# Kernel tuning notes

Measured on AMD Instinct MI355X. Metric: run time of the kernel, lower is better.

Reference implementation:

```python
import jax, jax.numpy as jnp
import numpy as np

B, G, GI = 128, 360, 174          # batch, n_groups, voxels per group
EF, ET, U = 512, 512, 512         # feat embed, text embed, LSTM units
AU, VOC, T = 32, 5000, 20         # attention units, vocab, max_len


def _leaky(x):
    return jnp.where(x >= 0, x, 0.2 * x)


def _ln(x, g, b, eps=1e-5):
    m = x.mean(-1, keepdims=True)
    v = ((x - m) ** 2).mean(-1, keepdims=True)
    return (x - m) / jnp.sqrt(v + eps) * g + b


def setup_inputs() -> dict:
    key = jax.random.key(0)
    ks = jax.random.split(key, 24)
    def n(k, shape, s=0.02):
        return jax.random.normal(k, shape, jnp.float32) * s
    return {
        "features": jax.random.normal(ks[0], (B, G * GI), jnp.float32),
        "text": jax.random.randint(ks[1], (B, T), 0, VOC),
        "a0": jnp.zeros((B, U), jnp.float32),
        "c0": jnp.zeros((B, U), jnp.float32),
        "enc_W": n(ks[2], (G, GI, EF)), "enc_b": n(ks[3], (G, EF)),
        "enc_ln_g": jnp.ones((EF,), jnp.float32), "enc_ln_b": jnp.zeros((EF,), jnp.float32),
        "attn_W1": n(ks[4], (EF, AU)), "attn_b1": n(ks[5], (AU,)),
        "attn_W2": n(ks[6], (U, AU)), "attn_b2": n(ks[7], (AU,)),
        "attn_V": n(ks[8], (AU, 1)), "attn_bV": n(ks[9], (1,)),
        "emb": n(ks[10], (VOC, ET)),
        "W_ih": n(ks[11], (4 * U, EF + ET)), "W_hh": n(ks[12], (4 * U, U)),
        "b_ih": n(ks[13], (4 * U,)), "b_hh": n(ks[14], (4 * U,)),
        "ln_g": jnp.ones((U,), jnp.float32), "ln_b": jnp.zeros((U,), jnp.float32),
        "dec_W1": n(ks[15], (U, 256)), "dec_b1": n(ks[16], (256,)),
        "dec_W2": n(ks[17], (256, VOC)), "dec_b2": n(ks[18], (VOC,)),
        "subject": 0,
    }


def reference(features, text, a0, c0, enc_W, enc_b, enc_ln_g, enc_ln_b,
              attn_W1, attn_b1, attn_W2, attn_b2, attn_V, attn_bV, emb,
              W_ih, W_hh, b_ih, b_hh, ln_g, ln_b,
              dec_W1, dec_b1, dec_W2, dec_b2, subject):
    # LocallyConnected encoder (weights for the selected subject): groups are
    # 360 contiguous equal splits of the voxel axis -> gather == reshape.
    x = features.reshape(B, G, GI)
    feat = _ln(_leaky(jnp.einsum('bgi,gio->bgo', x, enc_W) + enc_b),
               enc_ln_g, enc_ln_b)                       # [B, G, EF]
    # hidden-independent half of attention, hoisted out of the recurrence
    f1 = jax.nn.relu(jnp.einsum('bge,eu->bgu', feat, attn_W1) + attn_b1)  # [B,G,AU]
    txt = emb[text]                                      # [B, T, ET]

    def step(carry, x_t):
        a, c = carry                                     # [B,U], [B,U]
        h2 = jax.nn.relu(a @ attn_W2 + attn_b2)          # [B, AU]
        score = jnp.tanh(f1 + h2[:, None, :]) @ attn_V + attn_bV  # [B,G,1]
        w = jax.nn.softmax(score, axis=1)
        ctx = jnp.sum(w * feat, axis=1)                  # [B, EF]
        xin = jnp.concatenate([ctx, x_t], axis=1)        # [B, EF+ET]
        gates = xin @ W_ih.T + a @ W_hh.T + b_ih + b_hh  # [B, 4U]
        i, f, g, o = jnp.split(gates, 4, axis=1)         # torch gate order i,f,g,o
        c = jax.nn.sigmoid(f) * c + jax.nn.sigmoid(i) * jnp.tanh(g)
        h = jax.nn.sigmoid(o) * jnp.tanh(c)
        a = _ln(_leaky(h), ln_g, ln_b)                   # fed back as LSTM hidden
        out = jax.nn.softmax(_leaky(a @ dec_W1 + dec_b1) @ dec_W2 + dec_b2, axis=-1)
        return (a, c), (out, w)

    _, (outs, ws) = jax.lax.scan(step, (a0, c0), jnp.swapaxes(txt, 0, 1))
    output = jnp.swapaxes(outs, 0, 1)                    # [B, T, VOC]
    attention_scores = jnp.swapaxes(ws, 0, 1)            # [B, T, G, 1]
    return output, attention_scores
```

## Files before the change

### kernel.cpp

```cpp
#include <hip/hip_runtime.h>
#include <stdint.h>

#define B_  128
#define G_  360
#define GI_ 174
#define EF_ 512
#define U_  512
#define AU_ 32
#define VOC_ 5000
#define T_  20

typedef short short8 __attribute__((ext_vector_type(8)));
typedef float floatx4 __attribute__((ext_vector_type(4)));

#define GLD16(gp, lp) __builtin_amdgcn_global_load_lds( \
    (const __attribute__((address_space(1))) void*)(gp), \
    (__attribute__((address_space(3))) void*)(lp), 16, 0, 0)

__device__ __forceinline__ unsigned short f2bf(float f){
  unsigned u = __float_as_uint(f);
  u += 0x7fffu + ((u>>16)&1u);
  return (unsigned short)(u>>16);
}
__device__ __forceinline__ float2 bfpair(unsigned u){
  float2 r; r.x = __uint_as_float(u<<16); r.y = __uint_as_float(u & 0xffff0000u); return r;
}
__device__ __forceinline__ unsigned packbf(float a, float b){
  return ((unsigned)f2bf(b)<<16) | (unsigned)f2bf(a);
}
__device__ __forceinline__ float sigmf(float x){ return 1.0f/(1.0f + __expf(-x)); }
__device__ __forceinline__ float tanhf_(float x){ return 1.0f - 2.0f/(1.0f + __expf(2.0f*x)); }
__device__ __forceinline__ float leaky_(float x){ return x >= 0.f ? x : 0.2f*x; }

__device__ __forceinline__ int swzcol(int cc, int e){
  return (cc & ~63) | ((((cc>>3)&7) ^ e)<<3) | (cc&7);
}

__global__ __launch_bounds__(256) void k_cvt(
    const int* __restrict__ text, const float* __restrict__ emb,
    const float* __restrict__ Wih, const float* __restrict__ Whh,
    const float* __restrict__ bih, const float* __restrict__ bhh,
    const float* __restrict__ W1, const float* __restrict__ b1,
    const float* __restrict__ encg, const float* __restrict__ encb,
    const float* __restrict__ dW1, const float* __restrict__ dW2,
    float* __restrict__ stats, unsigned short* __restrict__ Wstep,
    float* __restrict__ bias_sum, unsigned short* __restrict__ ASbuf,
    unsigned short* __restrict__ W1g, float* __restrict__ f1c,
    unsigned short* __restrict__ dW1t, unsigned short* __restrict__ dW2t)
{
  __shared__ float tile[64][65];
  const int blk = blockIdx.x, tid = threadIdx.x;
  if (blk < 90){
    int i = blk*1024 + tid*4;
    *(float4*)&stats[i] = make_float4(0.f,0.f,0.f,0.f);
  } else if (blk < 2138){
    int j = blk - 90;
    #pragma unroll
    for (int q=0;q<6;++q){
      int c = q*256 + tid;
      float v;
      if (c < 512)       v = Wih[(size_t)j*1024 + 512 + c];
      else if (c < 1024) v = Wih[(size_t)j*1024 + (c - 512)];
      else               v = Whh[(size_t)j*512 + (c - 1024)];
      int cd = c;
      if (c >= 512) cd = 512 + swzcol(c - 512, j&7);
      Wstep[(size_t)j*1536 + cd] = f2bf(v);
    }
  } else if (blk < 2146){
    int i = (blk-2138)*256 + tid;
    bias_sum[i] = bih[i] + bhh[i];
  } else if (blk < 4706){
    int r = blk - 2146; int t = r >> 7, b = r & 127;
    int idx = text[b*T_ + t];
    float2 v = *(const float2*)&emb[(size_t)idx*512 + 2*tid];
    ((unsigned*)ASbuf)[(((size_t)r*1536)>>1) + tid] = packbf(v.x, v.y);
  } else if (blk == 4706){
    if (tid < 32){
      float gw = 0.f, bw = 0.f;
      for (int k=0;k<512;++k){
        float wv = W1[(size_t)k*32 + tid];
        float gk = encg[k], bk = encb[k];
        W1g[(size_t)tid*512 + k] = f2bf(gk*wv);
        gw += gk*wv; bw += bk*wv;
      }
      f1c[tid] = gw; f1c[32+tid] = bw + b1[tid];
    }
  } else if (blk < 4739){
    int q = blk - 4707; int kt = q >> 2, nt = q & 3;
    int k0 = kt*64, n0 = nt*64;
    #pragma unroll
    for (int it=0; it<16; ++it){
      int idx = it*256 + tid; int kk = idx>>6, nn = idx&63;
      tile[kk][nn] = dW1[(size_t)(k0+kk)*256 + n0+nn];
    }
    __syncthreads();
    #pragma unroll
    for (int it=0; it<16; ++it){
      int idx = it*256 + tid; int nn = idx>>6, kk = idx&63;
      dW1t[(size_t)(n0+nn)*512 + k0+kk] = f2bf(tile[kk][nn]);
    }
  } else {
    int q = blk - 4739; int kt = q/80, nt = q - kt*80;
    int k0 = kt*64, n0 = nt*64;
    #pragma unroll
    for (int it=0; it<16; ++it){
      int idx = it*256 + tid; int kk = idx>>6, nn = idx&63;
      tile[kk][nn] = (n0+nn < VOC_) ? dW2[(size_t)(k0+kk)*VOC_ + n0+nn] : 0.f;
    }
    __syncthreads();
    #pragma unroll
    for (int it=0; it<16; ++it){
      int idx = it*256 + tid; int nn = idx>>6, kk = idx&63;
      dW2t[(size_t)(n0+nn)*256 + k0+kk] = f2bf(tile[kk][nn]);
    }
  }
}

__device__ __forceinline__ int swz64(int row, int k){
  return row*64 + ((((k>>3) ^ (row&7)))<<3) + (k&7);
}
__global__ __launch_bounds__(256, 3) void k_enc(
    const float* __restrict__ features, const float* __restrict__ encW,
    const float* __restrict__ encB,
    unsigned short* __restrict__ ybuf, float* __restrict__ stats)
{
  __shared__ __align__(16) unsigned short As[128*64];
  __shared__ __align__(16) unsigned short Bs[128*64];
  const int g = blockIdx.y, n0 = blockIdx.x*128;
  const int tid = threadIdx.x, w = tid>>6, l = tid&63;
  const int quad = l>>4, col16 = l&15;
  const int m0w = (w>>1)*64, n0w = (w&1)*64;

  floatx4 acc[4][4];
  #pragma unroll
  for (int mi=0;mi<4;++mi)
    #pragma unroll
    for (int ni=0;ni<4;++ni)
      acc[mi][ni] = (floatx4){0.f,0.f,0.f,0.f};

  for (int c=0; c<3; ++c){
    if (c > 0) __syncthreads();
    #pragma unroll
    for (int q=0; q<8; ++q){
      int idx = q*256 + tid;
      int row = idx >> 4;
      int kq  = idx & 15;
      int kl  = kq*4;
      int kgl = c*64 + kl;
      const float* fp = features + (size_t)row*(G_*GI_) + (size_t)g*GI_ + kgl;
      float4 v;
      if (kgl + 3 < GI_){
        v = *(const float4*)fp;
      } else {
        v.x = (kgl+0 < GI_) ? fp[0] : 0.f;
        v.y = (kgl+1 < GI_) ? fp[1] : 0.f;
        v.z = (kgl+2 < GI_) ? fp[2] : 0.f;
        v.w = (kgl+3 < GI_) ? fp[3] : 0.f;
      }
      int e = row*64 + (((kl>>3) ^ (row&7))<<3) + (kl&7);
      uint2 pk; pk.x = packbf(v.x, v.y); pk.y = packbf(v.z, v.w);
      *(uint2*)&As[e] = pk;
    }
    #pragma unroll
    for (int zb=0; zb<2; ++zb){
      #pragma unroll
      for (int z=0; z<8; ++z){
        int zz = zb*8 + z;
        int kk = w + 4*zz;
        int k  = c*64 + kk;
        if (k < GI_){
          const float* wp = encW + ((size_t)g*GI_ + k)*512 + n0;
          float2 v = *(const float2*)&wp[2*l];
          Bs[swz64(2*l,   kk)] = f2bf(v.x);
          Bs[swz64(2*l+1, kk)] = f2bf(v.y);
        } else {
          Bs[swz64(2*l,   kk)] = 0;
          Bs[swz64(2*l+1, kk)] = 0;
        }
      }
    }
    __syncthreads();
    #pragma unroll
    for (int it=0; it<2; ++it){
      int kk = it*32 + quad*8;
      short8 af[4], bfr[4];
      #pragma unroll
      for (int mi=0;mi<4;++mi){
        int row = m0w + mi*16 + col16;
        af[mi] = *(const short8*)&As[row*64 + (((kk>>3) ^ (row&7))<<3)];
      }
      #pragma unroll
      for (int ni=0;ni<4;++ni){
        int rowb = n0w + ni*16 + col16;
        bfr[ni] = *(const short8*)&Bs[rowb*64 + (((kk>>3) ^ (rowb&7))<<3)];
      }
      #pragma unroll
      for (int mi=0;mi<4;++mi)
        #pragma unroll
        for (int ni=0;ni<4;++ni)
          acc[mi][ni] = __builtin_amdgcn_mfma_f32_16x16x32_bf16(af[mi], bfr[ni], acc[mi][ni], 0,0,0);
    }
  }

  #pragma unroll
  for (int mi=0;mi<4;++mi){
    float sy[4] = {0.f,0.f,0.f,0.f};
    float sq[4] = {0.f,0.f,0.f,0.f};
    #pragma unroll
    for (int ni=0;ni<4;++ni){
      int nG = n0 + n0w + ni*16 + col16;
      float bv = encB[(size_t)g*512 + nG];
      #pragma unroll
      for (int reg=0;reg<4;++reg){
        int row = m0w + mi*16 + quad*4 + reg;
        float y = leaky_(acc[mi][ni][reg] + bv);
        unsigned short yh = f2bf(y);
        ybuf[((size_t)row*G_ + g)*512 + nG] = yh;
        float yr = __uint_as_float(((unsigned)yh)<<16);
        sy[reg] += yr; sq[reg] += yr*yr;
      }
    }
    #pragma unroll
    for (int reg=0; reg<4; ++reg){
      float a = sy[reg], bq = sq[reg];
      #pragma unroll
      for (int mk=1; mk<16; mk<<=1){ a += __shfl_xor(a, mk, 64); bq += __shfl_xor(bq, mk, 64); }
      if (col16 == 0){
        int row = m0w + mi*16 + quad*4 + reg;
        atomicAdd(&stats[((size_t)row*G_ + g)*2],     a);
        atomicAdd(&stats[((size_t)row*G_ + g)*2 + 1], bq);
      }
    }
  }
}

template<int TN, int NBK, int MODE, int KSPLIT=1>
__global__ __launch_bounds__(256) void k_gemm(
    const unsigned short* __restrict__ A, int lda,
    const unsigned short* __restrict__ Bt, int ldb,
    const float* __restrict__ bias,
    float* __restrict__ outf, unsigned short* __restrict__ outh,
    const float* __restrict__ stats, float* __restrict__ stats2,
    const float* __restrict__ f1c)
{
  constexpr int NI = TN/32;
  __shared__ __align__(16) unsigned short As[128*64];
  __shared__ __align__(16) unsigned short Bs[TN*64];
  const int tid = threadIdx.x;
  const int w = tid >> 6, l = tid & 63;
  const int n0 = blockIdx.x * TN;
  const int ks = (KSPLIT > 1) ? blockIdx.y : 0;
  const int r0 = (KSPLIT > 1) ? 0 : blockIdx.y * 128;
  const int quad = l>>4, col16 = l&15;
  const int m0w = (w>>1)*64, n0w = (w&1)*(TN/2);
  const int arow = w*32, brow = w*(TN/4);

  const unsigned short* Ag = A + (size_t)(r0 + arow + (l>>3))*lda + (l&7)*8;
  const unsigned short* Bg = Bt + (size_t)(n0 + brow + (l>>3))*ldb + (l&7)*8;

  floatx4 acc[4][NI];
  #pragma unroll
  for (int mi=0;mi<4;++mi)
    #pragma unroll
    for (int ni=0;ni<NI;++ni)
      acc[mi][ni] = (floatx4){0.f,0.f,0.f,0.f};

  for (int it=0; it<NBK; ++it){
    int k0 = (ks*NBK + it)*64;
    #pragma unroll
    for (int q=0;q<4;++q)
      GLD16(Ag + (size_t)q*8*lda + k0, As + (arow + q*8)*64);
    #pragma unroll
    for (int q=0;q<TN/32;++q)
      GLD16(Bg + (size_t)q*8*ldb + k0, Bs + (brow + q*8)*64);
    __syncthreads();
    #pragma unroll
    for (int kc=0;kc<2;++kc){
      int koff = kc*32 + quad*8;
      short8 af[4], bfr[NI];
      #pragma unroll
      for (int mi=0;mi<4;++mi)
        af[mi] = *(const short8*)&As[(m0w + mi*16 + col16)*64 + koff];
      #pragma unroll
      for (int ni=0;ni<NI;++ni)
        bfr[ni] = *(const short8*)&Bs[(n0w + ni*16 + col16)*64 + koff];
      #pragma unroll
      for (int mi=0;mi<4;++mi)
        #pragma unroll
        for (int ni=0;ni<NI;++ni)
          acc[mi][ni] = __builtin_amdgcn_mfma_f32_16x16x32_bf16(af[mi], bfr[ni], acc[mi][ni], 0,0,0);
    }
    __syncthreads();
  }

  if constexpr (MODE == 0){
    float* op = outf + (size_t)ks*(128*2048);
    #pragma unroll
    for (int ni=0; ni<NI; ++ni){
      int nG = n0 + n0w + ni*16 + col16;
      float bv = (KSPLIT == 1 || ks == 0) ? bias[nG] : 0.f;
      #pragma unroll
      for (int mi=0; mi<4; ++mi)
        #pragma unroll
        for (int reg=0; reg<4; ++reg){
          int r = r0 + m0w + mi*16 + quad*4 + reg;
          op[(size_t)r*2048 + nG] = acc[mi][ni][reg] + bv;
        }
    }
  } else if constexpr (MODE == 1){
    int nG = n0w + col16;
    float gw = f1c[nG], bwv = f1c[32+nG];
    #pragma unroll
    for (int mi=0; mi<4; ++mi)
      #pragma unroll
      for (int reg=0; reg<4; ++reg){
        int r = r0 + m0w + mi*16 + quad*4 + reg;
        float2 st = *(const float2*)&stats[(size_t)r*2];
        float m = st.x * (1.f/512.f);
        float var = st.y * (1.f/512.f) - m*m;
        float rs = rsqrtf(var + 1e-5f);
        float v = rs*(acc[mi][0][reg] - m*gw) + bwv;
        v = v > 0.f ? v : 0.f;
        outf[(size_t)r*32 + nG] = v;
        if (((w&1)==0) && col16==0){
          stats2[(size_t)r*2] = m; stats2[(size_t)r*2+1] = rs;
        }
      }
  } else if constexpr (MODE == 2){
    #pragma unroll
    for (int ni=0; ni<NI; ++ni){
      int nG = n0 + n0w + ni*16 + col16;
      float bv = bias[nG];
      #pragma unroll
      for (int mi=0; mi<4; ++mi)
        #pragma unroll
        for (int reg=0; reg<4; ++reg){
          int r = r0 + m0w + mi*16 + quad*4 + reg;
          outh[(size_t)r*256 + nG] = f2bf(leaky_(acc[mi][ni][reg] + bv));
        }
    }
  } else {
    #pragma unroll
    for (int ni=0; ni<NI; ++ni){
      int nG = n0 + n0w + ni*16 + col16;
      if (nG < VOC_){
        float bv = bias[nG];
        #pragma unroll
        for (int mi=0; mi<4; ++mi)
          #pragma unroll
          for (int reg=0; reg<4; ++reg){
            int r = r0 + m0w + mi*16 + quad*4 + reg;
            int bb = r & 127, tt = r >> 7;
            outf[((size_t)bb*T_ + tt)*VOC_ + nG] = acc[mi][ni][reg] + bv;
          }
      }
    }
  }
}

__global__ __launch_bounds__(256) void k_gates(
    const unsigned short* __restrict__ A,
    const unsigned short* __restrict__ Bt,
    float* __restrict__ outp)
{
  __shared__ __align__(16) unsigned short As[128*128];
  __shared__ __align__(16) unsigned short Bs[64*128];
  const int tid = threadIdx.x, w = tid>>6, l = tid&63;
  const int ks = blockIdx.y;
  const int n0 = blockIdx.x*64;
  const int quad = l>>4, col16 = l&15;
  const int m0w = (w>>1)*64, n0w = (w&1)*32;
  const int arow = w*32, brow = w*16;

  const unsigned short* Ag = A + (size_t)(arow + (l>>4))*1536 + ks*128 + (l&15)*8;
  const unsigned short* Bg = Bt + (size_t)(n0 + brow + (l>>4))*1536 + 512 + ks*128 + (l&15)*8;
  #pragma unroll
  for (int q=0;q<8;++q)
    GLD16(Ag + (size_t)q*4*1536, As + (arow + q*4)*128);
  #pragma unroll
  for (int q=0;q<4;++q)
    GLD16(Bg + (size_t)q*4*1536, Bs + (brow + q*4)*128);

  floatx4 acc[4][2];
  #pragma unroll
  for (int mi=0;mi<4;++mi)
    #pragma unroll
    for (int ni=0;ni<2;++ni)
      acc[mi][ni] = (floatx4){0.f,0.f,0.f,0.f};

  __syncthreads();
  #pragma unroll
  for (int kc=0;kc<4;++kc){
    int koff = kc*32 + quad*8;
    int kbase = koff & 64;
    int kx = (koff>>3)&7;
    short8 af[4], bfr[2];
    #pragma unroll
    for (int mi=0;mi<4;++mi){
      int row = m0w + mi*16 + col16;
      af[mi] = *(const short8*)&As[row*128 + kbase + ((kx ^ (row&7))<<3)];
    }
    #pragma unroll
    for (int ni=0;ni<2;++ni){
      int rowb = n0w + ni*16 + col16;
      bfr[ni] = *(const short8*)&Bs[rowb*128 + kbase + ((kx ^ (rowb&7))<<3)];
    }
    #pragma unroll
    for (int mi=0;mi<4;++mi)
      #pragma unroll
      for (int ni=0;ni<2;++ni)
        acc[mi][ni] = __builtin_amdgcn_mfma_f32_16x16x32_bf16(af[mi], bfr[ni], acc[mi][ni], 0,0,0);
  }

  float* op = outp + (size_t)ks*(128*2048);
  #pragma unroll
  for (int ni=0; ni<2; ++ni){
    int nG = n0 + n0w + ni*16 + col16;
    #pragma unroll
    for (int mi=0; mi<4; ++mi)
      #pragma unroll
      for (int reg=0; reg<4; ++reg){
        int r = m0w + mi*16 + quad*4 + reg;
        op[(size_t)r*2048 + nG] = acc[mi][ni][reg];
      }
  }
}

__global__ __launch_bounds__(256) void k_cellattn(
    const float* __restrict__ gall, const float* __restrict__ gtx,
    const float* __restrict__ c_in,
    float* __restrict__ c_out, const float* __restrict__ a0,
    const float* __restrict__ lng, const float* __restrict__ lnb,
    const float* __restrict__ W2, const float* __restrict__ b2,
    const float* __restrict__ Vv, const float* __restrict__ bV,
    const float* __restrict__ f1, const unsigned short* __restrict__ ybuf,
    const float* __restrict__ stats2,
    const float* __restrict__ encg, const float* __restrict__ encb,
    unsigned short* __restrict__ ASlot, unsigned short* __restrict__ a_bf,
    float* __restrict__ att_out, int t_att, int mode_cell, int do_attn)
{
  __shared__ float a_s[512];
  __shared__ float sc[G_];
  __shared__ float hred[8*32];
  __shared__ float h2s[32];
  __shared__ float red[16];
  __shared__ float mrs[2];
  const int b = blockIdx.x, tid = threadIdx.x;
  const int wv = tid >> 6, ln = tid & 63;

  if (mode_cell){
    float hl2[2];
    #pragma unroll
    for (int q=0;q<2;++q){
      int u = tid + q*256;
      size_t base = (size_t)b*2048;
      float gi = gtx[base+u];
      float gf = gtx[base+512+u];
      float gc = gtx[base+1024+u];
      float go = gtx[base+1536+u];
      #pragma unroll
      for (int s=0;s<8;++s){
        const float* gp = gall + (size_t)s*(128*2048) + base;
        gi += gp[u]; gf += gp[512+u]; gc += gp[1024+u]; go += gp[1536+u];
      }
      float c = sigmf(gf)*c_in[(size_t)b*512+u] + sigmf(gi)*tanhf_(gc);
      c_out[(size_t)b*512+u] = c;
      hl2[q] = leaky_(sigmf(go)*tanhf_(c));
    }
    float s = hl2[0]+hl2[1], ss = hl2[0]*hl2[0]+hl2[1]*hl2[1];
    #pragma unroll
    for (int mk=1;mk<64;mk<<=1){ s += __shfl_xor(s,mk,64); ss += __shfl_xor(ss,mk,64); }
    if (ln==0){ red[wv]=s; red[8+wv]=ss; }
    __syncthreads();
    if (tid==0){
      float S  = red[0]+red[1]+red[2]+red[3];
      float SS = red[8]+red[9]+red[10]+red[11];
      float mean = S*(1.f/512.f);
      float var  = SS*(1.f/512.f) - mean*mean;
      mrs[0]=mean; mrs[1]=rsqrtf(var+1e-5f);
    }
    __syncthreads();
    float mean = mrs[0], rstd = mrs[1];
    #pragma unroll
    for (int q=0;q<2;++q){
      int u = tid + q*256;
      float av = (hl2[q]-mean)*rstd*lng[u] + lnb[u];
      a_s[u] = av;
      a_bf[(size_t)b*512 + u] = f2bf(av);
      if (do_attn){
        int pc = swzcol(512 + u, b&7);
        ASlot[(size_t)b*1536 + 512 + pc] = f2bf(av);
      }
    }
  } else {
    #pragma unroll
    for (int q=0;q<2;++q){
      int u = tid + q*256;
      float av = a0[(size_t)b*512 + u];
      a_s[u] = av;
      int pc = swzcol(512 + u, b&7);
      ASlot[(size_t)b*1536 + 512 + pc] = f2bf(av);
    }
  }
  __syncthreads();
  if (!do_attn) return;

  {
    int u = tid & 31, ch = tid >> 5;
    float p = 0.f;
    const float* w2p = W2 + (size_t)ch*64*32 + u;
    const float* ap = a_s + ch*64;
    #pragma unroll 8
    for (int e=0;e<64;++e) p += ap[e]*w2p[(size_t)e*32];
    hred[ch*32+u] = p;
  }
  __syncthreads();
  if (tid < 32){
    float p = hred[tid];
    #pragma unroll
    for (int ch=1; ch<8; ++ch) p += hred[ch*32+tid];
    p += b2[tid];
    h2s[tid] = p>0.f? p:0.f;
  }
  __syncthreads();
  float bVv = bV[0];
  for (int gg = tid; gg < G_; gg += 256){
    const float* fp = f1 + ((size_t)b*G_ + gg)*32;
    float s = bVv;
    #pragma unroll
    for (int u=0;u<32;++u) s += tanhf_(fp[u] + h2s[u]) * Vv[u];
    sc[gg] = s;
  }
  __syncthreads();
  float mx = -1e30f;
  for (int gg=tid; gg<G_; gg+=256) mx = fmaxf(mx, sc[gg]);
  #pragma unroll
  for (int mk=1;mk<64;mk<<=1) mx = fmaxf(mx, __shfl_xor(mx,mk,64));
  if (ln==0) red[wv]=mx;
  __syncthreads();
  if (tid==0) red[0] = fmaxf(fmaxf(red[0],red[1]),fmaxf(red[2],red[3]));
  __syncthreads();
  mx = red[0];
  float psum = 0.f;
  for (int gg=tid; gg<G_; gg+=256){
    float e = __expf(sc[gg]-mx);
    sc[gg] = e; psum += e;
  }
  #pragma unroll
  for (int mk=1;mk<64;mk<<=1) psum += __shfl_xor(psum,mk,64);
  if (ln==0) red[8+wv]=psum;
  __syncthreads();
  if (tid==0) red[8] = red[8]+red[9]+red[10]+red[11];
  __syncthreads();
  float inv = 1.f/red[8];
  float Mop = 0.f;
  float* wout = att_out + ((size_t)b*T_ + t_att)*G_;
  for (int gg=tid; gg<G_; gg+=256){
    float wg = sc[gg]*inv;
    wout[gg] = wg;
    float2 st = *(const float2*)&stats2[((size_t)b*G_+gg)*2];
    sc[gg] = wg*st.y;
    Mop += wg*st.x*st.y;
  }
  #pragma unroll
  for (int mk=1;mk<64;mk<<=1) Mop += __shfl_xor(Mop,mk,64);
  if (ln==0) red[4+wv] = Mop;
  __syncthreads();
  if (tid==0) mrs[0] = red[4]+red[5]+red[6]+red[7];
  __syncthreads();
  float Mo = mrs[0];
  {
    const unsigned* fp = (const unsigned*)ybuf + ((size_t)b*G_)*256 + tid;
    float c0v=0.f, c1v=0.f;
    for (int gg=0; gg<G_; ++gg){
      float2 p = bfpair(fp[(size_t)gg*256]);
      float wq = sc[gg];
      c0v += wq*p.x; c1v += wq*p.y;
    }
    int e0 = 2*tid;
    float ctx0 = encg[e0]  *(c0v - Mo) + encb[e0];
    float ctx1 = encg[e0+1]*(c1v - Mo) + encb[e0+1];
    int pc = swzcol(2*tid, b&7);
    ((unsigned*)ASlot)[((size_t)b*1536 + 512 + pc)>>1] = packbf(ctx0, ctx1);
  }
}

__global__ __launch_bounds__(256) void k_softmax(float* __restrict__ outp)
{
  __shared__ float red[8];
  const size_t row = (size_t)blockIdx.x * VOC_;
  const int tid = threadIdx.x;
  const int wv = tid >> 6, ln = tid & 63;
  float v[20];
  float mx = -1e30f;
  #pragma unroll
  for (int k=0;k<20;++k){
    int idx = tid + k*256;
    v[k] = (idx < VOC_) ? outp[row+idx] : -1e30f;
    mx = fmaxf(mx, v[k]);
  }
  #pragma unroll
  for (int mk=1;mk<64;mk<<=1) mx = fmaxf(mx,__shfl_xor(mx,mk,64));
  if (ln==0) red[wv] = mx;
  __syncthreads();
  if (tid==0) red[0]=fmaxf(fmaxf(red[0],red[1]),fmaxf(red[2],red[3]));
  __syncthreads();
  mx = red[0];
  float s=0.f;
  #pragma unroll
  for (int k=0;k<20;++k){ v[k] = __expf(v[k]-mx); s += v[k]; }
  #pragma unroll
  for (int mk=1;mk<64;mk<<=1) s += __shfl_xor(s,mk,64);
  if (ln==0) red[4+wv]=s;
  __syncthreads();
  if (tid==0) red[4]=red[4]+red[5]+red[6]+red[7];
  __syncthreads();
  float inv = 1.f/red[4];
  #pragma unroll
  for (int k=0;k<20;++k){
    int idx = tid + k*256;
    if (idx < VOC_) outp[row+idx] = v[k]*inv;
  }
}

extern "C" void kernel_launch(void* const* d_in, const int* in_sizes, int n_in,
                              void* d_out, int out_size, void* d_ws, size_t ws_size,
                              hipStream_t stream) {
  const float* features = (const float*)d_in[0];
  const int*   text     = (const int*)d_in[1];
  const float* a0    = (const float*)d_in[2];
  const float* c0    = (const float*)d_in[3];
  const float* encW  = (const float*)d_in[4];
  const float* encB  = (const float*)d_in[5];
  const float* encLNg= (const float*)d_in[6];
  const float* encLNb= (const float*)d_in[7];
  const float* attnW1= (const float*)d_in[8];
  const float* attnb1= (const float*)d_in[9];
  const float* attnW2= (const float*)d_in[10];
  const float* attnb2= (const float*)d_in[11];
  const float* attnV = (const float*)d_in[12];
  const float* attnbV= (const float*)d_in[13];
  const float* emb   = (const float*)d_in[14];
  const float* Wih   = (const float*)d_in[15];
  const float* Whh   = (const float*)d_in[16];
  const float* bih   = (const float*)d_in[17];
  const float* bhh   = (const float*)d_in[18];
  const float* lng   = (const float*)d_in[19];
  const float* lnb   = (const float*)d_in[20];
  const float* dW1   = (const float*)d_in[21];
  const float* db1   = (const float*)d_in[22];
  const float* dW2   = (const float*)d_in[23];
  const float* db2   = (const float*)d_in[24];

  uint8_t* w8 = (uint8_t*)d_ws;
  unsigned short* ybuf   = (unsigned short*)(w8);
  float*          stats  = (float*)(w8 + 47185920);
  float*          stats2 = (float*)(w8 + 47554560);
  float*          f1b    = (float*)(w8 + 47923200);
  unsigned short* ASbuf  = (unsigned short*)(w8 + 53821440);
  unsigned short* Wstep  = (unsigned short*)(w8 + 61685760);
  float*          bias_sum=(float*)(w8 + 67977216);
  unsigned short* W1g    = (unsigned short*)(w8 + 67985408);
  float*          f1c    = (float*)(w8 + 68018176);
  unsigned short* dW1t   = (unsigned short*)(w8 + 68018432);
  unsigned short* dW2t   = (unsigned short*)(w8 + 68280576);
  float*          cws    = (float*)(w8 + 71950592);
  unsigned short* a_bf   = (unsigned short*)(w8 + 72212736);
  unsigned short* d1bf   = (unsigned short*)(w8 + 74834176);

  float* outp = (float*)d_out;
  float* att  = outp + 12800000;
  float* gsplit = outp;
  float* gtxt   = outp + 8*128*2048;

  hipLaunchKernelGGL(k_cvt, dim3(5059), dim3(256), 0, stream,
                     text, emb, Wih, Whh, bih, bhh, attnW1, attnb1,
                     encLNg, encLNb, dW1, dW2,
                     stats, Wstep, bias_sum, ASbuf, W1g, f1c, dW1t, dW2t);
  hipLaunchKernelGGL(k_enc, dim3(4,360), dim3(256), 0, stream,
                     features, encW, encB, ybuf, stats);
  hipLaunchKernelGGL((k_gemm<64,8,0>), dim3(32,20), dim3(256), 0, stream,
                     ASbuf, 1536, Wstep, 1536, bias_sum,
                     gtxt, (unsigned short*)nullptr,
                     (const float*)nullptr, (float*)nullptr, (const float*)nullptr);
  hipLaunchKernelGGL((k_gemm<32,8,1>), dim3(1,360), dim3(256), 0, stream,
                     ybuf, 512, W1g, 512, (const float*)nullptr,
                     f1b, (unsigned short*)nullptr, stats, stats2, f1c);
  hipLaunchKernelGGL(k_cellattn, dim3(128), dim3(256), 0, stream,
                     gsplit, gtxt, c0, cws, a0, lng, lnb, attnW2, attnb2, attnV, attnbV,
                     f1b, ybuf, stats2, encLNg, encLNb,
                     ASbuf, a_bf, att, 0, 0, 1);
  for (int t=0; t<T_; ++t){
    hipLaunchKernelGGL(k_gates, dim3(32,8), dim3(256), 0, stream,
                       ASbuf + (size_t)t*128*1536 + 512, Wstep, gsplit);
    int da = (t < T_-1) ? 1 : 0;
    unsigned short* slot = ASbuf + (size_t)((t+1 < T_) ? (t+1) : 0)*128*1536;
    hipLaunchKernelGGL(k_cellattn, dim3(128), dim3(256), 0, stream,
                       gsplit, gtxt + (size_t)t*128*2048, (t==0)?c0:cws, cws, a0, lng, lnb,
                       attnW2, attnb2, attnV, attnbV,
                       f1b, ybuf, stats2, encLNg, encLNb,
                       slot, a_bf + (size_t)t*128*512, att, t+1, 1, da);
  }
  hipLaunchKernelGGL((k_gemm<128,8,2>), dim3(2,20), dim3(256), 0, stream,
                     a_bf, 512, dW1t, 512, db1,
                     (float*)nullptr, d1bf, (const float*)nullptr, (float*)nullptr,
                     (const float*)nullptr);
  hipLaunchKernelGGL((k_gemm<128,4,3>), dim3(40,20), dim3(256), 0, stream,
                     d1bf, 256, dW2t, 256, db2,
                     outp, (unsigned short*)nullptr, (const float*)nullptr,
                     (float*)nullptr, (const float*)nullptr);
  hipLaunchKernelGGL(k_softmax, dim3(2560), dim3(256), 0, stream, outp);
}
```

Baseline: 1.170 ms.

## Widen encoder blocks to 512 threads and split attention context over groups

The encoder GEMM kernel goes from 256 to 512 threads per block. Each wave now covers a 32x64 output sub-tile instead of 64x64, which halves the accumulator registers and raises wave parallelism for loading and MFMA. In the cell/attention kernel, the context reduction over 360 groups is split across the 4 waves, 90 groups each, with four columns per lane, and the partial sums are combined through shared memory. This shortens the serial dependency chain of the per-step context sum, at the cost of an extra shared buffer and a sync. The encoder epilogue that computes the stats reduction must still match the new wave layout, and that part is hidden.

```diff
diff --git a/kernel.cpp b/kernel.cpp
--- a/kernel.cpp
+++ b/kernel.cpp
@@ -119,7 +119,7 @@
 __device__ __forceinline__ int swz64(int row, int k){
   return row*64 + ((((k>>3) ^ (row&7)))<<3) + (k&7);
 }
-__global__ __launch_bounds__(256, 3) void k_enc(
+__global__ __launch_bounds__(512) void k_enc(
     const float* __restrict__ features, const float* __restrict__ encW,
     const float* __restrict__ encB,
     unsigned short* __restrict__ ybuf, float* __restrict__ stats)
@@ -129,11 +129,12 @@
   const int g = blockIdx.y, n0 = blockIdx.x*128;
   const int tid = threadIdx.x, w = tid>>6, l = tid&63;
   const int quad = l>>4, col16 = l&15;
-  const int m0w = (w>>1)*64, n0w = (w&1)*64;
-
-  floatx4 acc[4][4];
-  #pragma unroll
-  for (int mi=0;mi<4;++mi)
+  const int wm = w>>1, wn = w&1;
+  const int m0w = wm*32, n0w = wn*64;
+
+  floatx4 acc[2][4];
+  #pragma unroll
+  for (int mi=0;mi<2;++mi)
     #pragma unroll
     for (int ni=0;ni<4;++ni)
       acc[mi][ni] = (floatx4){0.f,0.f,0.f,0.f};
@@ -141,11 +142,10 @@
   for (int c=0; c<3; ++c){
     if (c > 0) __syncthreads();
     #pragma unroll
-    for (int q=0; q<8; ++q){
-      int idx = q*256 + tid;
+    for (int q=0; q<4; ++q){
+      int idx = q*512 + tid;
       int row = idx >> 4;
-      int kq  = idx & 15;
-      int kl  = kq*4;
+      int kl  = (idx & 15)*4;
       int kgl = c*64 + kl;
       const float* fp = features + (size_t)row*(G_*GI_) + (size_t)g*GI_ + kgl;
       float4 v;
@@ -162,30 +162,27 @@
       *(uint2*)&As[e] = pk;
     }
     #pragma unroll
-    for (int zb=0; zb<2; ++zb){
-      #pragma unroll
-      for (int z=0; z<8; ++z){
-        int zz = zb*8 + z;
-        int kk = w + 4*zz;
-        int k  = c*64 + kk;
-        if (k < GI_){
-          const float* wp = encW + ((size_t)g*GI_ + k)*512 + n0;
-          float2 v = *(const float2*)&wp[2*l];
-          Bs[swz64(2*l,   kk)] = f2bf(v.x);
-          Bs[swz64(2*l+1, kk)] = f2bf(v.y);
-        } else {
-          Bs[swz64(2*l,   kk)] = 0;
-          Bs[swz64(2*l+1, kk)] = 0;
-        }
+    for (int z=0; z<8; ++z){
+      int kk = (tid>>6) + 8*z;
+      int k  = c*64 + kk;
+      int nn = (tid&63)*2;
+      if (k < GI_){
+        const float* wp = encW + ((size_t)g*GI_ + k)*512 + n0 + nn;
+        float2 v = *(const float2*)wp;
+        Bs[swz64(nn,   kk)] = f2bf(v.x);
+        Bs[swz64(nn+1, kk)] = f2bf(v.y);
+      } else {
+        Bs[swz64(nn,   kk)] = 0;
+        Bs[swz64(nn+1, kk)] = 0;
       }
     }
     __syncthreads();
     #pragma unroll
     for (int it=0; it<2; ++it){
       int kk = it*32 + quad*8;
-      short8 af[4], bfr[4];
-      #pragma unroll
-      for (int mi=0;mi<4;++mi){
+      short8 af[2], bfr[4];
+      #pragma unroll
+      for (int mi=0;mi<2;++mi){
         int row = m0w + mi*16 + col16;
         af[mi] = *(const short8*)&As[row*64 + (((kk>>3) ^ (row&7))<<3)];
       }
@@ -195,7 +192,7 @@
         bfr[ni] = *(const short8*)&Bs[rowb*64 + (((kk>>3) ^ (rowb&7))<<3)];
       }
       #pragma unroll
-      for (int mi=0;mi<4;++mi)
+      for (int mi=0;mi<2;++mi)
         #pragma unroll
         for (int ni=0;ni<4;++ni)
           acc[mi][ni] = __builtin_amdgcn_mfma_f32_16x16x32_bf16(af[mi], bfr[ni], acc[mi][ni], 0,0,0);
@@ -203,7 +200,7 @@
   }
 
   #pragma unroll
-  for (int mi=0;mi<4;++mi){
+  for (int mi=0;mi<2;++mi){
     float sy[4] = {0.f,0.f,0.f,0.f};
     float sq[4] = {0.f,0.f,0.f,0.f};
     #pragma unroll
@@ -445,6 +442,7 @@
   __shared__ float h2s[32];
   __shared__ float red[16];
   __shared__ float mrs[2];
+  __shared__ float2 cred[4][256];
   const int b = blockIdx.x, tid = threadIdx.x;
   const int wv = tid >> 6, ln = tid & 63;
 
@@ -570,13 +568,26 @@
   __syncthreads();
   float Mo = mrs[0];
   {
-    const unsigned* fp = (const unsigned*)ybuf + ((size_t)b*G_)*256 + tid;
-    float c0v=0.f, c1v=0.f;
-    for (int gg=0; gg<G_; ++gg){
-      float2 p = bfpair(fp[(size_t)gg*256]);
+    const unsigned* fp = (const unsigned*)ybuf + ((size_t)b*G_)*256;
+    float2 cacc[4];
+    #pragma unroll
+    for (int k=0;k<4;++k) cacc[k] = make_float2(0.f,0.f);
+    int g0 = wv*90;
+    for (int gg=g0; gg<g0+90; ++gg){
       float wq = sc[gg];
-      c0v += wq*p.x; c1v += wq*p.y;
-    }
+      #pragma unroll
+      for (int k=0;k<4;++k){
+        float2 p = bfpair(fp[(size_t)gg*256 + ln + 64*k]);
+        cacc[k].x += wq*p.x; cacc[k].y += wq*p.y;
+      }
+    }
+    #pragma unroll
+    for (int k=0;k<4;++k) cred[wv][ln + 64*k] = cacc[k];
+  }
+  __syncthreads();
+  {
+    float c0v = cred[0][tid].x + cred[1][tid].x + cred[2][tid].x + cred[3][tid].x;
+    float c1v = cred[0][tid].y + cred[1][tid].y + cred[2][tid].y + cred[3][tid].y;
     int e0 = 2*tid;
     float ctx0 = encg[e0]  *(c0v - Mo) + encb[e0];
     float ctx1 = encg[e0+1]*(c1v - Mo) + encb[e0+1];
@@ -677,7 +688,7 @@
                      text, emb, Wih, Whh, bih, bhh, attnW1, attnb1,
                      encLNg, encLNb, dW1, dW2,
                      stats, Wstep, bias_sum, ASbuf, W1g, f1c, dW1t, dW2t);
-  hipLaunchKernelGGL(k_enc, dim3(4,360), dim3(256), 0, stream,
+  hipLaunchKernelGGL(k_enc, dim3(4,360), dim3(512), 0, stream,
                      features, encW, encB, ybuf, stats);
   hipLaunchKernelGGL((k_gemm<64,8,0>), dim3(32,20), dim3(256), 0, stream,
                      ASbuf, 1536, Wstep, 1536, bias_sum,
```

After: 1.011 ms. -13.5%, faster.
